# Optimization experiments

Hardware: AMD Instinct MI355X
Metric: run time of the kernel (lower is better)

Reference implementation:

```python
import jax, jax.numpy as jnp
import numpy as np

B = 1024          # batch
X = 32 * 32       # x_neuron_num
Y = 16384         # y_neuron_num (codebook size)
Z = 1000          # z_neuron_num (classes)
P_BU = 0.5        # y_bottom_up_percent


def _l2n(a, axis):
    # F.normalize: x / max(||x||, 1e-12)
    return a / jnp.maximum(jnp.linalg.norm(a, axis=axis, keepdims=True), 1e-12)


def setup_inputs() -> dict:
    key = jax.random.key(0)
    ks = jax.random.split(key, 8)
    return {
        "x": jax.random.normal(ks[0], (B, 32, 32), jnp.float32),
        "z": jax.random.randint(ks[1], (B,), 0, Z),
        "x2y_w": jax.random.uniform(ks[2], (Y, X), jnp.float32),
        "z2y_w": jax.random.uniform(ks[3], (Y, Z), jnp.float32),
        "y2z_w": jax.random.uniform(ks[4], (Z, Y), jnp.float32),
        "y_age": jax.random.randint(ks[5], (1, Y), 0, 5).astype(jnp.float32),
        "z_age": jax.random.randint(ks[6], (1, Z), 0, 5).astype(jnp.float32),
        "y_threshold": jax.random.uniform(ks[7], (1, Y), jnp.float32) * 0.5,
        "per_item": 1,
    }


def reference(x, z, x2y_w, z2y_w, y2z_w, y_age, z_age, y_threshold, per_item):
    # one 'train' step (torch forward returns inside the per_item loop)
    batch = x.shape[0]
    x = _l2n(x.reshape(batch, -1), 1)                 # [B, X]
    z_hot = jax.nn.one_hot(z, Z, dtype=x.dtype)       # normalized one-hot == one-hot
    Wx = _l2n(x2y_w, 1)                               # [Y, X]
    Wz = _l2n(z2y_w, 1)                               # [Y, Z]
    U = _l2n(y2z_w, 1)                                # [Z, Y]

    y_pre = P_BU * (x @ Wx.T) + (1.0 - P_BU) * (z_hot @ Wz.T)  # [B, Y]

    age = y_age[0]
    thr = y_threshold[0]
    max_resp = jnp.max(y_pre, axis=1)                 # [B]
    max_idx = jnp.argmax(y_pre, axis=1)               # [B]
    # age/threshold tie-break: losers re-argmax over unactivated neurons
    judge = (max_resp > thr[max_idx]) | (age[max_idx] < 1.0)
    unact = (age < 1.0).astype(y_pre.dtype)           # [Y]
    any_unact = jnp.sum(unact) > 0
    fallback = jnp.argmax(y_pre * unact[None, :], axis=1)
    max_idx = jnp.where(judge | ~any_unact, max_idx, fallback)

    # --- Hebbian update of x2y / z2y, expressed as segment reductions ---
    # torch dense form: sum_b y_lr[b,j]*(inp[b]-W[j]) / divisor_j
    ones_b = jnp.ones((batch,), x.dtype)
    cnt = jax.ops.segment_sum(ones_b, max_idx, num_segments=Y)       # [Y]
    div = jnp.where(cnt > 0, cnt, 1.0)
    lr = 1.0 / (age + 1.0)                                           # [Y]
    sumx = jax.ops.segment_sum(x, max_idx, num_segments=Y)           # [Y, X]
    Wx_new = Wx + (lr[:, None] * (sumx - cnt[:, None] * Wx)) / div[:, None]
    sumz = jax.ops.segment_sum(z_hot, max_idx, num_segments=Y)       # [Y, Z]
    Wz_new = Wz + (lr[:, None] * (sumz - cnt[:, None] * Wz)) / div[:, None]
    age_new = age + cnt

    # --- threshold update: per-winner min response (3 for non-winners) ---
    seg_min = jax.ops.segment_min(max_resp, max_idx, num_segments=Y)
    y_cur = jnp.minimum(seg_min, 3.0)
    y_cur = jnp.where(y_cur > 2.0, 0.0, y_cur)
    y_lr_eff = jnp.where(cnt > 0, lr, 0.0)   # sum_b y_lr[b,j]/divisor_j
    thr_new = y_lr_eff * y_cur + (1.0 - y_lr_eff) * thr

    # --- y2z update, segmented by label z ---
    zage = z_age[0]
    zlr = 1.0 / (zage + 1.0)                                          # [Z]
    y_resp = jax.nn.one_hot(max_idx, Y, dtype=x.dtype)                # [B, Y]
    cz = jax.ops.segment_sum(ones_b, z, num_segments=Z)               # [Z]
    dz = jnp.where(cz > 0, cz, 1.0)
    sumy = jax.ops.segment_sum(y_resp, z, num_segments=Z)             # [Z, Y]
    U_new = U + (zlr[:, None] * (sumy - cz[:, None] * U)) / dz[:, None]
    zage_new = zage + cz

    y_activated_num = jnp.sum((age_new >= 1.0).astype(jnp.int32))
    return (y_activated_num, max_resp, Wx_new, Wz_new, U_new,
            thr_new[None, :], age_new[None, :], zage_new[None, :])
```

## Files before the change

kernel.cpp:

```cpp
#include <hip/hip_runtime.h>

#define B_N 1024
#define X_N 1024
#define Y_N 16384
#define Z_N 1000
#define KD  1024
#define MARGIN 0.004f

#define OFF_ACT      0
#define OFF_MAXRESP  1
#define OFF_WX       1025
#define OFF_WZ       16778241
#define OFF_U        33162241
#define OFF_THR      49546241
#define OFF_AGE      49562625
#define OFF_ZAGE     49579009

#define SCR_B_BYTES    4112ull
#define SCR_S_BYTES    67112976ull
#define SCR_A_BYTES    132648976ull
#define SCR_CAND_BYTES 134746128ull
#define SCR_WZT_BYTES  136843280ull

#define WS_INV_X    0
#define WS_INV_WX   1024
#define WS_INV_WZ   17408
#define WS_FIDX     38912
#define WS_CNT      39936
#define WS_ZCNT     56320
#define WS_SEGMIN   57344
#define WS_CTR      73728
#define WS_MBITS    73736
#define WS_CCNT     74248

typedef unsigned short ushort_t;
typedef _Float16 f16x8 __attribute__((ext_vector_type(8)));
typedef float f32x4 __attribute__((ext_vector_type(4)));

__device__ __forceinline__ unsigned enc_f(float f) {
    unsigned u = __float_as_uint(f);
    return (u & 0x80000000u) ? ~u : (u | 0x80000000u);
}
__device__ __forceinline__ float dec_f(unsigned e) {
    unsigned u = (e & 0x80000000u) ? (e ^ 0x80000000u) : ~e;
    return __uint_as_float(u);
}
__device__ __forceinline__ unsigned long long pack_vi(float v, int y) {
    return ((unsigned long long)enc_f(v) << 32) |
           (unsigned long long)(0xFFFFFFFFu - (unsigned)y);
}
__device__ __forceinline__ ushort_t f2h(float f) {
    _Float16 h = (_Float16)f;
    ushort_t u; __builtin_memcpy(&u, &h, 2); return u;
}
__device__ __forceinline__ float h2f(unsigned lo16) {
    ushort_t u = (ushort_t)lo16; _Float16 h;
    __builtin_memcpy(&h, &u, 2); return (float)h;
}

#define GLOAD16(gp, lp) __builtin_amdgcn_global_load_lds( \
    (const __attribute__((address_space(1))) void*)(gp),  \
    (__attribute__((address_space(3))) void*)(lp), 16, 0, 0)

__global__ void init_kernel(int* cnt, unsigned* segmin, int* zcnt, int* ctr) {
    int i = blockIdx.x * 256 + threadIdx.x;
    if (i < Y_N) { cnt[i] = 0; segmin[i] = 0xFFFFFFFFu; }
    if (i < 1024) zcnt[i] = 0;
    if (i < 8) ctr[i] = (i == 2) ? 0x7FFFFFFF : 0;
}

__global__ void unact_kernel(const float* __restrict__ y_age, int* ctr,
                             unsigned long long* __restrict__ mbits) {
    int i = blockIdx.x * 256 + threadIdx.x;
    int a = (y_age[i] < 1.0f) ? 1 : 0;
    unsigned long long m = __ballot(a);
    int mi = a ? 0x7FFFFFFF : i;
    #pragma unroll
    for (int s = 32; s > 0; s >>= 1) mi = min(mi, __shfl_xor(mi, s, 64));
    if ((threadIdx.x & 63) == 0) {
        atomicAdd(ctr, (int)__popcll(m));
        mbits[i >> 6] = m;
        if (mi != 0x7FFFFFFF) atomicMin(&ctr[2], mi);
    }
}

__global__ __launch_bounds__(256) void pack_x_kernel(
    const float* __restrict__ x, ushort_t* __restrict__ A, float* __restrict__ inv_x) {
    const int b = blockIdx.x, t = threadIdx.x;
    const int lane = t & 63, wid = t >> 6;
    float4 v = reinterpret_cast<const float4*>(x + (size_t)b * X_N)[t];
    float ss = v.x*v.x + v.y*v.y + v.z*v.z + v.w*v.w;
    #pragma unroll
    for (int s = 32; s > 0; s >>= 1) ss += __shfl_xor(ss, s, 64);
    __shared__ float red[4];
    if (lane == 0) red[wid] = ss;
    __syncthreads();
    float inv = 1.0f / fmaxf(sqrtf(red[0] + red[1] + red[2] + red[3]), 1e-12f);
    if (t == 0) inv_x[b] = inv;
    ushort_t o1[4] = { f2h(v.x*inv), f2h(v.y*inv), f2h(v.z*inv), f2h(v.w*inv) };
    *reinterpret_cast<uint2*>(A + (size_t)b * KD + t * 4) = *reinterpret_cast<uint2*>(o1);
}

__global__ __launch_bounds__(256) void pack_w_kernel(
    const float* __restrict__ wxw, const float* __restrict__ wzw,
    ushort_t* __restrict__ Bm, float* __restrict__ inv_wx, float* __restrict__ inv_wz) {
    const int y = blockIdx.x, t = threadIdx.x;
    const int lane = t & 63, wid = t >> 6;
    float4 a = reinterpret_cast<const float4*>(wxw + (size_t)y * X_N)[t];
    float4 zv = make_float4(0.f, 0.f, 0.f, 0.f);
    if (t < 250) zv = reinterpret_cast<const float4*>(wzw + (size_t)y * Z_N)[t];
    float s1 = a.x*a.x + a.y*a.y + a.z*a.z + a.w*a.w;
    float s2 = zv.x*zv.x + zv.y*zv.y + zv.z*zv.z + zv.w*zv.w;
    #pragma unroll
    for (int s = 32; s > 0; s >>= 1) {
        s1 += __shfl_xor(s1, s, 64);
        s2 += __shfl_xor(s2, s, 64);
    }
    __shared__ float r1[4], r2[4];
    if (lane == 0) { r1[wid] = s1; r2[wid] = s2; }
    __syncthreads();
    float inv1 = 1.0f / fmaxf(sqrtf(r1[0] + r1[1] + r1[2] + r1[3]), 1e-12f);
    float inv2 = 1.0f / fmaxf(sqrtf(r2[0] + r2[1] + r2[2] + r2[3]), 1e-12f);
    ushort_t o1[4] = { f2h(a.x*inv1), f2h(a.y*inv1), f2h(a.z*inv1), f2h(a.w*inv1) };
    *reinterpret_cast<uint2*>(Bm + (size_t)y * KD + t * 4) = *reinterpret_cast<uint2*>(o1);
    if (t == 0) { inv_wx[y] = inv1; inv_wz[y] = inv2; }
}

__global__ __launch_bounds__(256) void wzt_kernel(
    const float* __restrict__ wzw, const float* __restrict__ inv_wz,
    ushort_t* __restrict__ wzt) {
    const int bid = blockIdx.x;
    const int z0 = (bid & 15) * 64, y0 = (bid >> 4) * 64;
    const int t = threadIdx.x;
    __shared__ float tile[64][65];
    #pragma unroll
    for (int p = 0; p < 4; ++p) {
        int yr = p * 16 + (t >> 4);
        int z = z0 + (t & 15) * 4;
        float4 v = make_float4(0.f, 0.f, 0.f, 0.f);
        if (z + 3 < Z_N)
            v = *reinterpret_cast<const float4*>(wzw + (size_t)(y0 + yr) * Z_N + z);
        float s = 0.5f * inv_wz[y0 + yr];
        tile[(t & 15) * 4 + 0][yr] = v.x * s;
        tile[(t & 15) * 4 + 1][yr] = v.y * s;
        tile[(t & 15) * 4 + 2][yr] = v.z * s;
        tile[(t & 15) * 4 + 3][yr] = v.w * s;
    }
    __syncthreads();
    #pragma unroll
    for (int p = 0; p < 4; ++p) {
        int zr = p * 16 + (t >> 4);
        int yc = (t & 15) * 4;
        if (z0 + zr < 1024) {
            ushort_t o[4] = { f2h(tile[zr][yc]), f2h(tile[zr][yc + 1]),
                              f2h(tile[zr][yc + 2]), f2h(tile[zr][yc + 3]) };
            *reinterpret_cast<uint2*>(wzt + (size_t)(z0 + zr) * Y_N + y0 + yc) =
                *reinterpret_cast<uint2*>(o);
        }
    }
}

__global__ __launch_bounds__(512, 1) void mm256_kernel(const ushort_t* __restrict__ A,
                                                       const ushort_t* __restrict__ Bm,
                                                       ushort_t* __restrict__ S) {
    __shared__ __align__(16) _Float16 lds[4][2][1024][8];
    const int t = threadIdx.x;
    const int wid = t >> 6, lane = t & 63;
    const int bid = blockIdx.x;
    const int lb = (bid & 7) * 32 + (bid >> 3);
    const int mt = lb & 3, nt = lb >> 2;
    const int b0 = mt * 256, y0 = nt * 256;
    const int wr = wid >> 2, wc = wid & 3;
    const int r = lane & 15, gq = lane >> 4;
    const int NK = KD / 32;

    f32x4 acc[8][4];
    #pragma unroll
    for (int i = 0; i < 8; ++i)
        #pragma unroll
        for (int j = 0; j < 4; ++j) acc[i][j] = (f32x4){0.f, 0.f, 0.f, 0.f};

    auto stage = [&](int buf, int k0) {
        #pragma unroll
        for (int rr = 0; rr < 2; ++rr) {
            int s = rr * 512 + t;
            int row = s & 255, g = s >> 8;
            GLOAD16(A  + (size_t)(b0 + row) * KD + k0 + g * 8, &lds[buf][0][s][0]);
            GLOAD16(Bm + (size_t)(y0 + row) * KD + k0 + g * 8, &lds[buf][1][s][0]);
        }
    };

    stage(0, 0);
    stage(1, 32);
    stage(2, 64);
    asm volatile("s_waitcnt vmcnt(8)" ::: "memory");
    __builtin_amdgcn_s_barrier();
    asm volatile("" ::: "memory");

    for (int ks = 0; ks < NK; ++ks) {
        const int cur = ks & 3;
        f16x8 bF[4];
        #pragma unroll
        for (int nf = 0; nf < 4; ++nf)
            bF[nf] = *reinterpret_cast<const f16x8*>(
                &lds[cur][1][gq * 256 + wc * 64 + nf * 16 + r][0]);
        __builtin_amdgcn_s_setprio(1);
        #pragma unroll
        for (int mf = 0; mf < 8; ++mf) {
            f16x8 aF = *reinterpret_cast<const f16x8*>(
                &lds[cur][0][gq * 256 + wr * 128 + mf * 16 + r][0]);
            #pragma unroll
            for (int nf = 0; nf < 4; ++nf)
                acc[mf][nf] = __builtin_amdgcn_mfma_f32_16x16x32_f16(
                    aF, bF[nf], acc[mf][nf], 0, 0, 0);
        }
        __builtin_amdgcn_s_setprio(0);
        if (ks == NK - 1) break;

        __builtin_amdgcn_s_barrier();
        asm volatile("" ::: "memory");
        if (ks + 3 < NK) {
            stage((ks + 3) & 3, (ks + 3) * 32);
            asm volatile("s_waitcnt vmcnt(8)" ::: "memory");
        } else if (ks + 3 == NK) {
            asm volatile("s_waitcnt vmcnt(4)" ::: "memory");
        } else {
            asm volatile("s_waitcnt vmcnt(0)" ::: "memory");
        }
        __builtin_amdgcn_s_barrier();
        asm volatile("" ::: "memory");
    }

    #pragma unroll
    for (int mf = 0; mf < 8; ++mf) {
        int bg = b0 + wr * 128 + mf * 16 + gq * 4;
        #pragma unroll
        for (int nf = 0; nf < 4; ++nf) {
            int yg = y0 + wc * 64 + nf * 16 + r;
            f32x4 c = acc[mf][nf];
            #pragma unroll
            for (int q = 0; q < 4; ++q)
                S[(size_t)(bg + q) * Y_N + yg] = f2h(0.5f * c[q]);
        }
    }
}

__global__ __launch_bounds__(256) void scan_kernel(
    const ushort_t* __restrict__ scores, const ushort_t* __restrict__ wzt,
    const int* __restrict__ zlab, const unsigned long long* __restrict__ mbits,
    const int* __restrict__ ctr, unsigned* __restrict__ gcand, int* __restrict__ ccnt) {
    const int b = blockIdx.x, t = threadIdx.x;
    const int lane = t & 63, wid = t >> 6;
    const uint4* srow = reinterpret_cast<const uint4*>(scores + (size_t)b * Y_N);
    const uint4* wrow = reinterpret_cast<const uint4*>(wzt + (size_t)zlab[b] * Y_N);

    float vmax = -1e30f, mmax = -1e30f;
    for (int c = t; c < Y_N / 8; c += 256) {
        uint4 pk = srow[c];
        uint4 wz = wrow[c];
        int yb = c * 8;
        unsigned m8 = (unsigned)((mbits[yb >> 6] >> (yb & 63)) & 0xFFull);
        unsigned w[4] = {pk.x, pk.y, pk.z, pk.w};
        unsigned q[4] = {wz.x, wz.y, wz.z, wz.w};
        #pragma unroll
        for (int j = 0; j < 4; ++j) {
            float v0 = h2f(w[j] & 0xFFFFu) + h2f(q[j] & 0xFFFFu);
            float v1 = h2f(w[j] >> 16) + h2f(q[j] >> 16);
            vmax = fmaxf(vmax, fmaxf(v0, v1));
            mmax = fmaxf(mmax, v0 * (float)((m8 >> (2 * j)) & 1u));
            mmax = fmaxf(mmax, v1 * (float)((m8 >> (2 * j + 1)) & 1u));
        }
    }
    #pragma unroll
    for (int s = 32; s > 0; s >>= 1) {
        vmax = fmaxf(vmax, __shfl_xor(vmax, s, 64));
        mmax = fmaxf(mmax, __shfl_xor(mmax, s, 64));
    }
    __shared__ float rv[4], rm[4];
    __shared__ int nA_s, nB_s;
    __shared__ int cA[256], cB[256];
    if (lane == 0) { rv[wid] = vmax; rm[wid] = mmax; }
    if (t == 0) { nA_s = 0; nB_s = 0; }
    __syncthreads();
    float tA = fmaxf(fmaxf(rv[0], rv[1]), fmaxf(rv[2], rv[3])) - MARGIN;
    float tB = fmaxf(fmaxf(rm[0], rm[1]), fmaxf(rm[2], rm[3])) - MARGIN;
    bool anyu = ctr[0] > 0;

    for (int c = t; c < Y_N / 8; c += 256) {
        uint4 pk = srow[c];
        uint4 wz = wrow[c];
        int yb = c * 8;
        unsigned m8 = (unsigned)((mbits[yb >> 6] >> (yb & 63)) & 0xFFull);
        unsigned w[4] = {pk.x, pk.y, pk.z, pk.w};
        unsigned q[4] = {wz.x, wz.y, wz.z, wz.w};
        #pragma unroll
        for (int j = 0; j < 8; ++j) {
            unsigned sw = (j & 1) ? (w[j >> 1] >> 16) : (w[j >> 1] & 0xFFFFu);
            unsigned qw = (j & 1) ? (q[j >> 1] >> 16) : (q[j >> 1] & 0xFFFFu);
            float v = h2f(sw) + h2f(qw);
            if (v >= tA) { int p = atomicAdd(&nA_s, 1); if (p < 256) cA[p] = yb + j; }
            if (anyu && ((m8 >> j) & 1u) && v >= tB) {
                int p = atomicAdd(&nB_s, 1); if (p < 256) cB[p] = yb + j;
            }
        }
    }
    __syncthreads();
    int nA = min(nA_s, 256), nB = min(nB_s, 256);
    unsigned* slab = gcand + (size_t)b * 512;
    for (int i = t; i < nA; i += 256) slab[i] = (unsigned)cA[i];
    for (int i = t; i < nB; i += 256) slab[256 + i] = (unsigned)cB[i];
    if (t == 0) ccnt[b] = nA | (nB << 16);
}

__global__ __launch_bounds__(256) void rescore_kernel(
    const unsigned* __restrict__ gcand, const int* __restrict__ ccnt,
    const float* __restrict__ x, const float* __restrict__ inv_x,
    const float* __restrict__ wxw, const float* __restrict__ inv_wx,
    const float* __restrict__ wzw, const float* __restrict__ inv_wz,
    const int* __restrict__ zlab, const float* __restrict__ y_thr,
    const float* __restrict__ y_age, const int* __restrict__ ctr,
    int* final_idx, int* cnt, unsigned* segmin, int* zcnt,
    float* __restrict__ out_maxresp) {
    const int b = blockIdx.x, t = threadIdx.x;
    const int lane = t & 63, wid = t >> 6;
    int pc = ccnt[b];
    int nA = pc & 0xFFFF, nB = pc >> 16;
    int zb = zlab[b];
    float invx = inv_x[b];
    const unsigned* slab = gcand + (size_t)b * 512;

    const float4* xr = reinterpret_cast<const float4*>(x + (size_t)b * X_N);
    float4 xv[4];
    #pragma unroll
    for (int j = 0; j < 4; ++j) xv[j] = xr[j * 64 + lane];

    __shared__ unsigned long long red[4];
    __shared__ unsigned long long sPM;
    __shared__ int sTakeA;

    unsigned long long bA = 0ull;
    for (int c = wid; c < nA; c += 8) {
        int y1 = (int)slab[c];
        int c2 = c + 4;
        bool h2 = c2 < nA;
        int y2 = (int)slab[h2 ? c2 : c];
        const float4* w1 = reinterpret_cast<const float4*>(wxw + (size_t)y1 * X_N);
        const float4* w2 = reinterpret_cast<const float4*>(wxw + (size_t)y2 * X_N);
        float d1 = 0.f, d2 = 0.f;
        #pragma unroll
        for (int j = 0; j < 4; ++j) {
            float4 a1 = w1[j * 64 + lane];
            float4 a2 = w2[j * 64 + lane];
            d1 += xv[j].x*a1.x + xv[j].y*a1.y + xv[j].z*a1.z + xv[j].w*a1.w;
            d2 += xv[j].x*a2.x + xv[j].y*a2.y + xv[j].z*a2.z + xv[j].w*a2.w;
        }
        #pragma unroll
        for (int s = 32; s > 0; s >>= 1) {
            d1 += __shfl_xor(d1, s, 64);
            d2 += __shfl_xor(d2, s, 64);
        }
        float v1 = 0.5f*invx*inv_wx[y1]*d1 + 0.5f*inv_wz[y1]*wzw[(size_t)y1*Z_N + zb];
        unsigned long long p1 = pack_vi(v1, y1);
        bA = (p1 > bA) ? p1 : bA;
        if (h2) {
            float v2 = 0.5f*invx*inv_wx[y2]*d2 + 0.5f*inv_wz[y2]*wzw[(size_t)y2*Z_N + zb];
            unsigned long long p2 = pack_vi(v2, y2);
            bA = (p2 > bA) ? p2 : bA;
        }
    }
    if (lane == 0) red[wid] = bA;
    __syncthreads();
    if (t == 0) {
        unsigned long long pm = red[0];
        #pragma unroll
        for (int j = 1; j < 4; ++j) pm = (red[j] > pm) ? red[j] : pm;
        sPM = pm;
        unsigned enc = (unsigned)(pm >> 32);
        int idx = (int)(0xFFFFFFFFu - (unsigned)(pm & 0xFFFFFFFFull));
        float mresp = dec_f(enc);
        out_maxresp[b] = mresp;
        bool judge = (mresp > y_thr[idx]) || (y_age[idx] < 1.0f);
        bool anyu = ctr[0] > 0;
        sTakeA = (judge || !anyu) ? 1 : 0;
    }
    __syncthreads();

    if (!sTakeA) {
        unsigned long long bB = 0ull;
        for (int c = wid; c < nB; c += 8) {
            int y1 = (int)slab[256 + c];
            int c2 = c + 4;
            bool h2 = c2 < nB;
            int y2 = (int)slab[256 + (h2 ? c2 : c)];
            const float4* w1 = reinterpret_cast<const float4*>(wxw + (size_t)y1 * X_N);
            const float4* w2 = reinterpret_cast<const float4*>(wxw + (size_t)y2 * X_N);
            float d1 = 0.f, d2 = 0.f;
            #pragma unroll
            for (int j = 0; j < 4; ++j) {
                float4 a1 = w1[j * 64 + lane];
                float4 a2 = w2[j * 64 + lane];
                d1 += xv[j].x*a1.x + xv[j].y*a1.y + xv[j].z*a1.z + xv[j].w*a1.w;
                d2 += xv[j].x*a2.x + xv[j].y*a2.y + xv[j].z*a2.z + xv[j].w*a2.w;
            }
            #pragma unroll
            for (int s = 32; s > 0; s >>= 1) {
                d1 += __shfl_xor(d1, s, 64);
                d2 += __shfl_xor(d2, s, 64);
            }
            float v1 = 0.5f*invx*inv_wx[y1]*d1 + 0.5f*inv_wz[y1]*wzw[(size_t)y1*Z_N + zb];
            unsigned long long p1 = pack_vi(v1, y1);
            bB = (p1 > bB) ? p1 : bB;
            if (h2) {
                float v2 = 0.5f*invx*inv_wx[y2]*d2 + 0.5f*inv_wz[y2]*wzw[(size_t)y2*Z_N + zb];
                unsigned long long p2 = pack_vi(v2, y2);
                bB = (p2 > bB) ? p2 : bB;
            }
        }
        if (lane == 0) red[wid] = bB;
    }
    __syncthreads();
    if (t == 0) {
        unsigned long long pm = sPM;
        unsigned enc = (unsigned)(pm >> 32);
        int idx = (int)(0xFFFFFFFFu - (unsigned)(pm & 0xFFFFFFFFull));
        int fin;
        if (sTakeA) {
            fin = idx;
        } else if (nB > 0) {
            unsigned long long pf = red[0];
            #pragma unroll
            for (int j = 1; j < 4; ++j) pf = (red[j] > pf) ? red[j] : pf;
            fin = (int)(0xFFFFFFFFu - (unsigned)(pf & 0xFFFFFFFFull));
        } else {
            fin = ctr[2];
        }
        final_idx[b] = fin;
        atomicAdd(&cnt[fin], 1);
        atomicMin(&segmin[fin], enc);
        atomicAdd(&zcnt[zb], 1);
    }
}

__global__ __launch_bounds__(256) void wx_out_kernel(
    const float* __restrict__ wxw, const float* __restrict__ inv_wx,
    const float* __restrict__ x, const float* __restrict__ inv_x,
    const int* __restrict__ final_idx, const int* __restrict__ cnt,
    const float* __restrict__ y_age, float* __restrict__ outw) {
    int j = blockIdx.x;
    int t = threadIdx.x;
    __shared__ int s_b[1024];
    __shared__ int s_n;
    if (t == 0) s_n = 0;
    __syncthreads();
    int c = cnt[j];
    if (c > 0) {
        for (int b = t; b < B_N; b += 256)
            if (final_idx[b] == j) { int p = atomicAdd(&s_n, 1); s_b[p] = b; }
    }
    __syncthreads();
    float inv = inv_wx[j];
    float lr = 1.0f / (y_age[j] + 1.0f);
    float fc = (float)c;
    float dv = (c > 0) ? fc : 1.0f;
    int n = s_n;
    float4 w = *reinterpret_cast<const float4*>(wxw + (size_t)j * X_N + t * 4);
    float4 wn = make_float4(w.x*inv, w.y*inv, w.z*inv, w.w*inv);
    if (c > 0) {
        float4 s = make_float4(0.f, 0.f, 0.f, 0.f);
        for (int m = 0; m < n; ++m) {
            int b = s_b[m];
            float ix = inv_x[b];
            float4 xv = *reinterpret_cast<const float4*>(x + (size_t)b * X_N + t * 4);
            s.x += xv.x * ix; s.y += xv.y * ix; s.z += xv.z * ix; s.w += xv.w * ix;
        }
        float f = lr / dv;
        wn.x += f * (s.x - fc * wn.x);
        wn.y += f * (s.y - fc * wn.y);
        wn.z += f * (s.z - fc * wn.z);
        wn.w += f * (s.w - fc * wn.w);
    }
    *reinterpret_cast<float4*>(outw + (size_t)j * X_N + t * 4) = wn;
}

__global__ __launch_bounds__(256) void wz_out_kernel(
    const float* __restrict__ wzw, const float* __restrict__ inv_wz,
    const int* __restrict__ zlab, const int* __restrict__ final_idx,
    const int* __restrict__ cnt, const float* __restrict__ y_age,
    float* __restrict__ outw) {
    int j = blockIdx.x;
    int t = threadIdx.x;
    __shared__ int s_c[1024];
    __shared__ int s_n;
    if (t == 0) s_n = 0;
    __syncthreads();
    int c = cnt[j];
    if (c > 0) {
        for (int b = t; b < B_N; b += 256)
            if (final_idx[b] == j) { int p = atomicAdd(&s_n, 1); s_c[p] = zlab[b]; }
    }
    __syncthreads();
    if (t >= 250) return;
    float inv = inv_wz[j];
    float lr = 1.0f / (y_age[j] + 1.0f);
    float fc = (float)c;
    float dv = (c > 0) ? fc : 1.0f;
    int n = s_n;
    float4 w = *reinterpret_cast<const float4*>(wzw + (size_t)j * Z_N + t * 4);
    float4 wn = make_float4(w.x*inv, w.y*inv, w.z*inv, w.w*inv);
    if (c > 0) {
        float4 s = make_float4(0.f, 0.f, 0.f, 0.f);
        for (int m = 0; m < n; ++m) {
            int d = s_c[m] - t * 4;
            if (d == 0) s.x += 1.f;
            else if (d == 1) s.y += 1.f;
            else if (d == 2) s.z += 1.f;
            else if (d == 3) s.w += 1.f;
        }
        float f = lr / dv;
        wn.x += f * (s.x - fc * wn.x);
        wn.y += f * (s.y - fc * wn.y);
        wn.z += f * (s.z - fc * wn.z);
        wn.w += f * (s.w - fc * wn.w);
    }
    *reinterpret_cast<float4*>(outw + (size_t)j * Z_N + t * 4) = wn;
}

__global__ __launch_bounds__(256) void u_out_kernel(
    const float* __restrict__ uw, const int* __restrict__ zlab,
    const int* __restrict__ final_idx, const int* __restrict__ zcnt,
    const float* __restrict__ z_age, float* __restrict__ outw) {
    int cz = blockIdx.x;
    int t = threadIdx.x;
    const int lane = t & 63, wid = t >> 6;
    __shared__ int s_w[1024];
    __shared__ int s_n;
    __shared__ float rss[4];
    if (t == 0) s_n = 0;

    const float4* rowp4 = reinterpret_cast<const float4*>(uw + (size_t)cz * Y_N);
    float4 u[16];
    float ss = 0.f;
    #pragma unroll
    for (int p = 0; p < 16; ++p) {
        u[p] = rowp4[p * 256 + t];
        ss += u[p].x*u[p].x + u[p].y*u[p].y + u[p].z*u[p].z + u[p].w*u[p].w;
    }
    #pragma unroll
    for (int s = 32; s > 0; s >>= 1) ss += __shfl_xor(ss, s, 64);
    if (lane == 0) rss[wid] = ss;
    __syncthreads();
    float inv = 1.0f / fmaxf(sqrtf(rss[0] + rss[1] + rss[2] + rss[3]), 1e-12f);

    int c = zcnt[cz];
    if (c > 0) {
        for (int b = t; b < B_N; b += 256)
            if (zlab[b] == cz) { int p = atomicAdd(&s_n, 1); s_w[p] = final_idx[b]; }
    }
    __syncthreads();
    float zlr = 1.0f / (z_age[cz] + 1.0f);
    float fc = (float)c;
    float dv = (c > 0) ? fc : 1.0f;
    float f = zlr / dv;
    int n = s_n;
    float* outp = outw + (size_t)cz * Y_N;
    #pragma unroll
    for (int p = 0; p < 16; ++p) {
        int e4 = p * 256 + t;
        float4 un = make_float4(u[p].x*inv, u[p].y*inv, u[p].z*inv, u[p].w*inv);
        if (c > 0) {
            float4 s = make_float4(0.f, 0.f, 0.f, 0.f);
            for (int m = 0; m < n; ++m) {
                int d = s_w[m] - e4 * 4;
                if (d == 0) s.x += 1.f;
                else if (d == 1) s.y += 1.f;
                else if (d == 2) s.z += 1.f;
                else if (d == 3) s.w += 1.f;
            }
            un.x += f * (s.x - fc * un.x);
            un.y += f * (s.y - fc * un.y);
            un.z += f * (s.z - fc * un.z);
            un.w += f * (s.w - fc * un.w);
        }
        *reinterpret_cast<float4*>(outp + e4 * 4) = un;
    }
}

__global__ void thr_age_kernel(const int* __restrict__ cnt, const unsigned* __restrict__ segmin,
                               const float* __restrict__ y_age, const float* __restrict__ y_thr,
                               float* __restrict__ out_thr, float* __restrict__ out_age,
                               int* ctr) {
    int j = blockIdx.x * 256 + threadIdx.x;
    int c = cnt[j];
    float age = y_age[j];
    float thr = y_thr[j];
    float tn = thr;
    if (c > 0) {
        float lr = 1.0f / (age + 1.0f);
        float smin = dec_f(segmin[j]);
        float ycur = fminf(smin, 3.0f);
        if (ycur > 2.0f) ycur = 0.0f;
        tn = lr * ycur + (1.0f - lr) * thr;
    }
    out_thr[j] = tn;
    float an = age + (float)c;
    out_age[j] = an;
    unsigned long long m = __ballot(an >= 1.0f ? 1 : 0);
    if ((threadIdx.x & 63) == 0) atomicAdd(ctr + 1, (int)__popcll(m));
}

__global__ void zage_act_kernel(const int* __restrict__ zcnt, const float* __restrict__ z_age,
                                const int* __restrict__ ctr, float* __restrict__ out_zage,
                                float* __restrict__ out_act) {
    int i = blockIdx.x * 256 + threadIdx.x;
    if (i < Z_N) out_zage[i] = z_age[i] + (float)zcnt[i];
    if (i == 0) out_act[0] = (float)ctr[1];
}

extern "C" void kernel_launch(void* const* d_in, const int* in_sizes, int n_in,
                              void* d_out, int out_size, void* d_ws, size_t ws_size,
                              hipStream_t stream) {
    const float* x     = (const float*)d_in[0];
    const int*   z     = (const int*)d_in[1];
    const float* wxw   = (const float*)d_in[2];
    const float* wzw   = (const float*)d_in[3];
    const float* uw    = (const float*)d_in[4];
    const float* y_age = (const float*)d_in[5];
    const float* z_age = (const float*)d_in[6];
    const float* y_thr = (const float*)d_in[7];
    float* out = (float*)d_out;
    float* ws  = (float*)d_ws;
    char*  ob  = (char*)d_out;

    float* inv_x  = ws + WS_INV_X;
    float* inv_wx = ws + WS_INV_WX;
    float* inv_wz = ws + WS_INV_WZ;
    int* fidx = (int*)(ws + WS_FIDX);
    int* cnt  = (int*)(ws + WS_CNT);
    int* zcnt = (int*)(ws + WS_ZCNT);
    unsigned* segmin = (unsigned*)(ws + WS_SEGMIN);
    int* ctr = (int*)(ws + WS_CTR);
    unsigned long long* mbits = (unsigned long long*)(ws + WS_MBITS);
    int* ccnt = (int*)(ws + WS_CCNT);

    ushort_t* Bb  = (ushort_t*)(ob + SCR_B_BYTES);
    ushort_t* Sc  = (ushort_t*)(ob + SCR_S_BYTES);
    ushort_t* Ab  = (ushort_t*)(ob + SCR_A_BYTES);
    unsigned* gcand = (unsigned*)(ob + SCR_CAND_BYTES);
    ushort_t* wzt = (ushort_t*)(ob + SCR_WZT_BYTES);

    init_kernel<<<64, 256, 0, stream>>>(cnt, segmin, zcnt, ctr);
    unact_kernel<<<Y_N / 256, 256, 0, stream>>>(y_age, ctr, mbits);
    pack_x_kernel<<<B_N, 256, 0, stream>>>(x, Ab, inv_x);
    pack_w_kernel<<<Y_N, 256, 0, stream>>>(wxw, wzw, Bb, inv_wx, inv_wz);
    wzt_kernel<<<16 * 256, 256, 0, stream>>>(wzw, inv_wz, wzt);
    mm256_kernel<<<(B_N / 256) * (Y_N / 256), 512, 0, stream>>>(Ab, Bb, Sc);
    scan_kernel<<<B_N, 256, 0, stream>>>(Sc, wzt, z, mbits, ctr, gcand, ccnt);
    rescore_kernel<<<B_N, 256, 0, stream>>>(gcand, ccnt, x, inv_x, wxw, inv_wx, wzw, inv_wz,
                                            z, y_thr, y_age, ctr, fidx, cnt, segmin, zcnt,
                                            out + OFF_MAXRESP);
    wx_out_kernel<<<Y_N, 256, 0, stream>>>(wxw, inv_wx, x, inv_x, fidx, cnt, y_age, out + OFF_WX);
    wz_out_kernel<<<Y_N, 256, 0, stream>>>(wzw, inv_wz, z, fidx, cnt, y_age, out + OFF_WZ);
    u_out_kernel<<<Z_N, 256, 0, stream>>>(uw, z, fidx, zcnt, z_age, out + OFF_U);
    thr_age_kernel<<<Y_N / 256, 256, 0, stream>>>(cnt, segmin, y_age, y_thr,
                                                  out + OFF_THR, out + OFF_AGE, ctr);
    zage_act_kernel<<<4, 256, 0, stream>>>(zcnt, z_age, ctr, out + OFF_ZAGE, out + OFF_ACT);
}
```

Before: 259.0 us.

## Fuse prep, scan/rescore and output kernels to cut launches and scratch traffic

Three groups of kernels are merged into block-indexed fused kernels. The unact, pack_x and pack_w work becomes one prep kernel. The scan and rescore kernels become one kernel that keeps candidate lists in shared memory instead of a global slab. The wx/wz/u output updates and the thr/age/zage work become one out kernel, and the activated-count write moves to a tiny final kernel. The aim is to remove per-launch gaps and tail serialization, and to skip the global candidate write and read. The trade-off is larger kernels with more shared memory and registers, which could lower occupancy, and heterogeneous block types whose run times differ.

```diff
diff --git a/kernel.cpp b/kernel.cpp
--- a/kernel.cpp
+++ b/kernel.cpp
@@ -19,7 +19,6 @@
 #define SCR_B_BYTES    4112ull
 #define SCR_S_BYTES    67112976ull
 #define SCR_A_BYTES    132648976ull
-#define SCR_CAND_BYTES 134746128ull
 #define SCR_WZT_BYTES  136843280ull
 
 #define WS_INV_X    0
@@ -31,7 +30,6 @@
 #define WS_SEGMIN   57344
 #define WS_CTR      73728
 #define WS_MBITS    73736
-#define WS_CCNT     74248
 
 typedef unsigned short ushort_t;
 typedef _Float16 f16x8 __attribute__((ext_vector_type(8)));
@@ -69,61 +67,59 @@
     if (i < 8) ctr[i] = (i == 2) ? 0x7FFFFFFF : 0;
 }
 
-__global__ void unact_kernel(const float* __restrict__ y_age, int* ctr,
-                             unsigned long long* __restrict__ mbits) {
-    int i = blockIdx.x * 256 + threadIdx.x;
-    int a = (y_age[i] < 1.0f) ? 1 : 0;
-    unsigned long long m = __ballot(a);
-    int mi = a ? 0x7FFFFFFF : i;
-    #pragma unroll
-    for (int s = 32; s > 0; s >>= 1) mi = min(mi, __shfl_xor(mi, s, 64));
-    if ((threadIdx.x & 63) == 0) {
-        atomicAdd(ctr, (int)__popcll(m));
-        mbits[i >> 6] = m;
-        if (mi != 0x7FFFFFFF) atomicMin(&ctr[2], mi);
-    }
-}
-
-__global__ __launch_bounds__(256) void pack_x_kernel(
-    const float* __restrict__ x, ushort_t* __restrict__ A, float* __restrict__ inv_x) {
-    const int b = blockIdx.x, t = threadIdx.x;
-    const int lane = t & 63, wid = t >> 6;
-    float4 v = reinterpret_cast<const float4*>(x + (size_t)b * X_N)[t];
-    float ss = v.x*v.x + v.y*v.y + v.z*v.z + v.w*v.w;
-    #pragma unroll
-    for (int s = 32; s > 0; s >>= 1) ss += __shfl_xor(ss, s, 64);
-    __shared__ float red[4];
-    if (lane == 0) red[wid] = ss;
-    __syncthreads();
-    float inv = 1.0f / fmaxf(sqrtf(red[0] + red[1] + red[2] + red[3]), 1e-12f);
-    if (t == 0) inv_x[b] = inv;
-    ushort_t o1[4] = { f2h(v.x*inv), f2h(v.y*inv), f2h(v.z*inv), f2h(v.w*inv) };
-    *reinterpret_cast<uint2*>(A + (size_t)b * KD + t * 4) = *reinterpret_cast<uint2*>(o1);
-}
-
-__global__ __launch_bounds__(256) void pack_w_kernel(
+__global__ __launch_bounds__(256) void prep_kernel(
+    const float* __restrict__ y_age, int* ctr, unsigned long long* __restrict__ mbits,
+    const float* __restrict__ x, ushort_t* __restrict__ A, float* __restrict__ inv_x,
     const float* __restrict__ wxw, const float* __restrict__ wzw,
     ushort_t* __restrict__ Bm, float* __restrict__ inv_wx, float* __restrict__ inv_wz) {
-    const int y = blockIdx.x, t = threadIdx.x;
+    const int bid = blockIdx.x, t = threadIdx.x;
     const int lane = t & 63, wid = t >> 6;
-    float4 a = reinterpret_cast<const float4*>(wxw + (size_t)y * X_N)[t];
-    float4 zv = make_float4(0.f, 0.f, 0.f, 0.f);
-    if (t < 250) zv = reinterpret_cast<const float4*>(wzw + (size_t)y * Z_N)[t];
-    float s1 = a.x*a.x + a.y*a.y + a.z*a.z + a.w*a.w;
-    float s2 = zv.x*zv.x + zv.y*zv.y + zv.z*zv.z + zv.w*zv.w;
-    #pragma unroll
-    for (int s = 32; s > 0; s >>= 1) {
-        s1 += __shfl_xor(s1, s, 64);
-        s2 += __shfl_xor(s2, s, 64);
-    }
-    __shared__ float r1[4], r2[4];
-    if (lane == 0) { r1[wid] = s1; r2[wid] = s2; }
-    __syncthreads();
-    float inv1 = 1.0f / fmaxf(sqrtf(r1[0] + r1[1] + r1[2] + r1[3]), 1e-12f);
-    float inv2 = 1.0f / fmaxf(sqrtf(r2[0] + r2[1] + r2[2] + r2[3]), 1e-12f);
-    ushort_t o1[4] = { f2h(a.x*inv1), f2h(a.y*inv1), f2h(a.z*inv1), f2h(a.w*inv1) };
-    *reinterpret_cast<uint2*>(Bm + (size_t)y * KD + t * 4) = *reinterpret_cast<uint2*>(o1);
-    if (t == 0) { inv_wx[y] = inv1; inv_wz[y] = inv2; }
+    __shared__ float red1[4], red2[4];
+
+    if (bid < 64) {
+        int i = bid * 256 + t;
+        int a = (y_age[i] < 1.0f) ? 1 : 0;
+        unsigned long long m = __ballot(a);
+        int mi = a ? 0x7FFFFFFF : i;
+        #pragma unroll
+        for (int s = 32; s > 0; s >>= 1) mi = min(mi, __shfl_xor(mi, s, 64));
+        if (lane == 0) {
+            atomicAdd(ctr, (int)__popcll(m));
+            mbits[i >> 6] = m;
+            if (mi != 0x7FFFFFFF) atomicMin(&ctr[2], mi);
+        }
+    } else if (bid < 64 + B_N) {
+        int b = bid - 64;
+        float4 v = reinterpret_cast<const float4*>(x + (size_t)b * X_N)[t];
+        float ss = v.x*v.x + v.y*v.y + v.z*v.z + v.w*v.w;
+        #pragma unroll
+        for (int s = 32; s > 0; s >>= 1) ss += __shfl_xor(ss, s, 64);
+        if (lane == 0) red1[wid] = ss;
+        __syncthreads();
+        float inv = 1.0f / fmaxf(sqrtf(red1[0] + red1[1] + red1[2] + red1[3]), 1e-12f);
+        if (t == 0) inv_x[b] = inv;
+        ushort_t o1[4] = { f2h(v.x*inv), f2h(v.y*inv), f2h(v.z*inv), f2h(v.w*inv) };
+        *reinterpret_cast<uint2*>(A + (size_t)b * KD + t * 4) = *reinterpret_cast<uint2*>(o1);
+    } else {
+        int y = bid - 64 - B_N;
+        float4 a = reinterpret_cast<const float4*>(wxw + (size_t)y * X_N)[t];
+        float4 zv = make_float4(0.f, 0.f, 0.f, 0.f);
+        if (t < 250) zv = reinterpret_cast<const float4*>(wzw + (size_t)y * Z_N)[t];
+        float s1 = a.x*a.x + a.y*a.y + a.z*a.z + a.w*a.w;
+        float s2 = zv.x*zv.x + zv.y*zv.y + zv.z*zv.z + zv.w*zv.w;
+        #pragma unroll
+        for (int s = 32; s > 0; s >>= 1) {
+            s1 += __shfl_xor(s1, s, 64);
+            s2 += __shfl_xor(s2, s, 64);
+        }
+        if (lane == 0) { red1[wid] = s1; red2[wid] = s2; }
+        __syncthreads();
+        float inv1 = 1.0f / fmaxf(sqrtf(red1[0] + red1[1] + red1[2] + red1[3]), 1e-12f);
+        float inv2 = 1.0f / fmaxf(sqrtf(red2[0] + red2[1] + red2[2] + red2[3]), 1e-12f);
+        ushort_t o1[4] = { f2h(a.x*inv1), f2h(a.y*inv1), f2h(a.z*inv1), f2h(a.w*inv1) };
+        *reinterpret_cast<uint2*>(Bm + (size_t)y * KD + t * 4) = *reinterpret_cast<uint2*>(o1);
+        if (t == 0) { inv_wx[y] = inv1; inv_wz[y] = inv2; }
+    }
 }
 
 __global__ __launch_bounds__(256) void wzt_kernel(
@@ -245,14 +241,28 @@
     }
 }
 
-__global__ __launch_bounds__(256) void scan_kernel(
+__global__ __launch_bounds__(256) void scanres_kernel(
     const ushort_t* __restrict__ scores, const ushort_t* __restrict__ wzt,
     const int* __restrict__ zlab, const unsigned long long* __restrict__ mbits,
-    const int* __restrict__ ctr, unsigned* __restrict__ gcand, int* __restrict__ ccnt) {
+    const int* __restrict__ ctr,
+    const float* __restrict__ x, const float* __restrict__ inv_x,
+    const float* __restrict__ wxw, const float* __restrict__ inv_wx,
+    const float* __restrict__ wzw, const float* __restrict__ inv_wz,
+    const float* __restrict__ y_thr, const float* __restrict__ y_age,
+    int* final_idx, int* cnt, unsigned* segmin, int* zcnt,
+    float* __restrict__ out_maxresp) {
     const int b = blockIdx.x, t = threadIdx.x;
     const int lane = t & 63, wid = t >> 6;
+    const int zb = zlab[b];
     const uint4* srow = reinterpret_cast<const uint4*>(scores + (size_t)b * Y_N);
-    const uint4* wrow = reinterpret_cast<const uint4*>(wzt + (size_t)zlab[b] * Y_N);
+    const uint4* wrow = reinterpret_cast<const uint4*>(wzt + (size_t)zb * Y_N);
+
+    __shared__ float rv[4], rm[4];
+    __shared__ int nA_s, nB_s;
+    __shared__ int cA[256], cB[256];
+    __shared__ unsigned long long red[4];
+    __shared__ unsigned long long sPM;
+    __shared__ int sTakeA;
 
     float vmax = -1e30f, mmax = -1e30f;
     for (int c = t; c < Y_N / 8; c += 256) {
@@ -276,9 +286,6 @@
         vmax = fmaxf(vmax, __shfl_xor(vmax, s, 64));
         mmax = fmaxf(mmax, __shfl_xor(mmax, s, 64));
     }
-    __shared__ float rv[4], rm[4];
-    __shared__ int nA_s, nB_s;
-    __shared__ int cA[256], cB[256];
     if (lane == 0) { rv[wid] = vmax; rm[wid] = mmax; }
     if (t == 0) { nA_s = 0; nB_s = 0; }
     __syncthreads();
@@ -306,44 +313,19 @@
     }
     __syncthreads();
     int nA = min(nA_s, 256), nB = min(nB_s, 256);
-    unsigned* slab = gcand + (size_t)b * 512;
-    for (int i = t; i < nA; i += 256) slab[i] = (unsigned)cA[i];
-    for (int i = t; i < nB; i += 256) slab[256 + i] = (unsigned)cB[i];
-    if (t == 0) ccnt[b] = nA | (nB << 16);
-}
-
-__global__ __launch_bounds__(256) void rescore_kernel(
-    const unsigned* __restrict__ gcand, const int* __restrict__ ccnt,
-    const float* __restrict__ x, const float* __restrict__ inv_x,
-    const float* __restrict__ wxw, const float* __restrict__ inv_wx,
-    const float* __restrict__ wzw, const float* __restrict__ inv_wz,
-    const int* __restrict__ zlab, const float* __restrict__ y_thr,
-    const float* __restrict__ y_age, const int* __restrict__ ctr,
-    int* final_idx, int* cnt, unsigned* segmin, int* zcnt,
-    float* __restrict__ out_maxresp) {
-    const int b = blockIdx.x, t = threadIdx.x;
-    const int lane = t & 63, wid = t >> 6;
-    int pc = ccnt[b];
-    int nA = pc & 0xFFFF, nB = pc >> 16;
-    int zb = zlab[b];
+
     float invx = inv_x[b];
-    const unsigned* slab = gcand + (size_t)b * 512;
-
     const float4* xr = reinterpret_cast<const float4*>(x + (size_t)b * X_N);
     float4 xv[4];
     #pragma unroll
     for (int j = 0; j < 4; ++j) xv[j] = xr[j * 64 + lane];
 
-    __shared__ unsigned long long red[4];
-    __shared__ unsigned long long sPM;
-    __shared__ int sTakeA;
-
     unsigned long long bA = 0ull;
     for (int c = wid; c < nA; c += 8) {
-        int y1 = (int)slab[c];
+        int y1 = cA[c];
         int c2 = c + 4;
         bool h2 = c2 < nA;
-        int y2 = (int)slab[h2 ? c2 : c];
+        int y2 = cA[h2 ? c2 : c];
         const float4* w1 = reinterpret_cast<const float4*>(wxw + (size_t)y1 * X_N);
         const float4* w2 = reinterpret_cast<const float4*>(wxw + (size_t)y2 * X_N);
         float d1 = 0.f, d2 = 0.f;
@@ -380,7 +362,6 @@
         float mresp = dec_f(enc);
         out_maxresp[b] = mresp;
         bool judge = (mresp > y_thr[idx]) || (y_age[idx] < 1.0f);
-        bool anyu = ctr[0] > 0;
         sTakeA = (judge || !anyu) ? 1 : 0;
     }
     __syncthreads();
@@ -388,10 +369,10 @@
     if (!sTakeA) {
         unsigned long long bB = 0ull;
         for (int c = wid; c < nB; c += 8) {
-            int y1 = (int)slab[256 + c];
+            int y1 = cB[c];
             int c2 = c + 4;
             bool h2 = c2 < nB;
-            int y2 = (int)slab[256 + (h2 ? c2 : c)];
+            int y2 = cB[h2 ? c2 : c];
             const float4* w1 = reinterpret_cast<const float4*>(wxw + (size_t)y1 * X_N);
             const float4* w2 = reinterpret_cast<const float4*>(wxw + (size_t)y2 * X_N);
             float d1 = 0.f, d2 = 0.f;
@@ -441,179 +422,161 @@
     }
 }
 
-__global__ __launch_bounds__(256) void wx_out_kernel(
+__global__ __launch_bounds__(256) void out_kernel(
     const float* __restrict__ wxw, const float* __restrict__ inv_wx,
     const float* __restrict__ x, const float* __restrict__ inv_x,
+    const float* __restrict__ wzw, const float* __restrict__ inv_wz,
+    const float* __restrict__ uw, const int* __restrict__ zlab,
     const int* __restrict__ final_idx, const int* __restrict__ cnt,
-    const float* __restrict__ y_age, float* __restrict__ outw) {
-    int j = blockIdx.x;
-    int t = threadIdx.x;
-    __shared__ int s_b[1024];
-    __shared__ int s_n;
-    if (t == 0) s_n = 0;
-    __syncthreads();
-    int c = cnt[j];
-    if (c > 0) {
-        for (int b = t; b < B_N; b += 256)
-            if (final_idx[b] == j) { int p = atomicAdd(&s_n, 1); s_b[p] = b; }
-    }
-    __syncthreads();
-    float inv = inv_wx[j];
-    float lr = 1.0f / (y_age[j] + 1.0f);
-    float fc = (float)c;
-    float dv = (c > 0) ? fc : 1.0f;
-    int n = s_n;
-    float4 w = *reinterpret_cast<const float4*>(wxw + (size_t)j * X_N + t * 4);
-    float4 wn = make_float4(w.x*inv, w.y*inv, w.z*inv, w.w*inv);
-    if (c > 0) {
-        float4 s = make_float4(0.f, 0.f, 0.f, 0.f);
-        for (int m = 0; m < n; ++m) {
-            int b = s_b[m];
-            float ix = inv_x[b];
-            float4 xv = *reinterpret_cast<const float4*>(x + (size_t)b * X_N + t * 4);
-            s.x += xv.x * ix; s.y += xv.y * ix; s.z += xv.z * ix; s.w += xv.w * ix;
-        }
-        float f = lr / dv;
-        wn.x += f * (s.x - fc * wn.x);
-        wn.y += f * (s.y - fc * wn.y);
-        wn.z += f * (s.z - fc * wn.z);
-        wn.w += f * (s.w - fc * wn.w);
-    }
-    *reinterpret_cast<float4*>(outw + (size_t)j * X_N + t * 4) = wn;
-}
-
-__global__ __launch_bounds__(256) void wz_out_kernel(
-    const float* __restrict__ wzw, const float* __restrict__ inv_wz,
-    const int* __restrict__ zlab, const int* __restrict__ final_idx,
-    const int* __restrict__ cnt, const float* __restrict__ y_age,
-    float* __restrict__ outw) {
-    int j = blockIdx.x;
-    int t = threadIdx.x;
-    __shared__ int s_c[1024];
-    __shared__ int s_n;
-    if (t == 0) s_n = 0;
-    __syncthreads();
-    int c = cnt[j];
-    if (c > 0) {
-        for (int b = t; b < B_N; b += 256)
-            if (final_idx[b] == j) { int p = atomicAdd(&s_n, 1); s_c[p] = zlab[b]; }
-    }
-    __syncthreads();
-    if (t >= 250) return;
-    float inv = inv_wz[j];
-    float lr = 1.0f / (y_age[j] + 1.0f);
-    float fc = (float)c;
-    float dv = (c > 0) ? fc : 1.0f;
-    int n = s_n;
-    float4 w = *reinterpret_cast<const float4*>(wzw + (size_t)j * Z_N + t * 4);
-    float4 wn = make_float4(w.x*inv, w.y*inv, w.z*inv, w.w*inv);
-    if (c > 0) {
-        float4 s = make_float4(0.f, 0.f, 0.f, 0.f);
-        for (int m = 0; m < n; ++m) {
-            int d = s_c[m] - t * 4;
-            if (d == 0) s.x += 1.f;
-            else if (d == 1) s.y += 1.f;
-            else if (d == 2) s.z += 1.f;
-            else if (d == 3) s.w += 1.f;
-        }
-        float f = lr / dv;
-        wn.x += f * (s.x - fc * wn.x);
-        wn.y += f * (s.y - fc * wn.y);
-        wn.z += f * (s.z - fc * wn.z);
-        wn.w += f * (s.w - fc * wn.w);
-    }
-    *reinterpret_cast<float4*>(outw + (size_t)j * Z_N + t * 4) = wn;
-}
-
-__global__ __launch_bounds__(256) void u_out_kernel(
-    const float* __restrict__ uw, const int* __restrict__ zlab,
-    const int* __restrict__ final_idx, const int* __restrict__ zcnt,
-    const float* __restrict__ z_age, float* __restrict__ outw) {
-    int cz = blockIdx.x;
-    int t = threadIdx.x;
+    const int* __restrict__ zcnt, const unsigned* __restrict__ segmin,
+    const float* __restrict__ y_age, const float* __restrict__ z_age,
+    const float* __restrict__ y_thr, float* __restrict__ out, int* ctr) {
+    const int bid = blockIdx.x, t = threadIdx.x;
     const int lane = t & 63, wid = t >> 6;
-    __shared__ int s_w[1024];
+    __shared__ int s_idx[1024];
     __shared__ int s_n;
     __shared__ float rss[4];
-    if (t == 0) s_n = 0;
-
-    const float4* rowp4 = reinterpret_cast<const float4*>(uw + (size_t)cz * Y_N);
-    float4 u[16];
-    float ss = 0.f;
-    #pragma unroll
-    for (int p = 0; p < 16; ++p) {
-        u[p] = rowp4[p * 256 + t];
-        ss += u[p].x*u[p].x + u[p].y*u[p].y + u[p].z*u[p].z + u[p].w*u[p].w;
-    }
-    #pragma unroll
-    for (int s = 32; s > 0; s >>= 1) ss += __shfl_xor(ss, s, 64);
-    if (lane == 0) rss[wid] = ss;
-    __syncthreads();
-    float inv = 1.0f / fmaxf(sqrtf(rss[0] + rss[1] + rss[2] + rss[3]), 1e-12f);
-
-    int c = zcnt[cz];
-    if (c > 0) {
-        for (int b = t; b < B_N; b += 256)
-            if (zlab[b] == cz) { int p = atomicAdd(&s_n, 1); s_w[p] = final_idx[b]; }
-    }
-    __syncthreads();
-    float zlr = 1.0f / (z_age[cz] + 1.0f);
-    float fc = (float)c;
-    float dv = (c > 0) ? fc : 1.0f;
-    float f = zlr / dv;
-    int n = s_n;
-    float* outp = outw + (size_t)cz * Y_N;
-    #pragma unroll
-    for (int p = 0; p < 16; ++p) {
-        int e4 = p * 256 + t;
-        float4 un = make_float4(u[p].x*inv, u[p].y*inv, u[p].z*inv, u[p].w*inv);
+
+    if (bid < Z_N) {
+        int cz = bid;
+        if (t == 0) s_n = 0;
+        const float4* rowp4 = reinterpret_cast<const float4*>(uw + (size_t)cz * Y_N);
+        float4 u[16];
+        float ss = 0.f;
+        #pragma unroll
+        for (int p = 0; p < 16; ++p) {
+            u[p] = rowp4[p * 256 + t];
+            ss += u[p].x*u[p].x + u[p].y*u[p].y + u[p].z*u[p].z + u[p].w*u[p].w;
+        }
+        #pragma unroll
+        for (int s = 32; s > 0; s >>= 1) ss += __shfl_xor(ss, s, 64);
+        if (lane == 0) rss[wid] = ss;
+        __syncthreads();
+        float inv = 1.0f / fmaxf(sqrtf(rss[0] + rss[1] + rss[2] + rss[3]), 1e-12f);
+        int c = zcnt[cz];
+        if (c > 0) {
+            for (int b = t; b < B_N; b += 256)
+                if (zlab[b] == cz) { int p = atomicAdd(&s_n, 1); s_idx[p] = final_idx[b]; }
+        }
+        __syncthreads();
+        float zlr = 1.0f / (z_age[cz] + 1.0f);
+        float fc = (float)c;
+        float dv = (c > 0) ? fc : 1.0f;
+        float f = zlr / dv;
+        int n = s_n;
+        float* outp = out + OFF_U + (size_t)cz * Y_N;
+        #pragma unroll
+        for (int p = 0; p < 16; ++p) {
+            int e4 = p * 256 + t;
+            float4 un = make_float4(u[p].x*inv, u[p].y*inv, u[p].z*inv, u[p].w*inv);
+            if (c > 0) {
+                float4 s = make_float4(0.f, 0.f, 0.f, 0.f);
+                for (int m = 0; m < n; ++m) {
+                    int d = s_idx[m] - e4 * 4;
+                    if (d == 0) s.x += 1.f;
+                    else if (d == 1) s.y += 1.f;
+                    else if (d == 2) s.z += 1.f;
+                    else if (d == 3) s.w += 1.f;
+                }
+                un.x += f * (s.x - fc * un.x);
+                un.y += f * (s.y - fc * un.y);
+                un.z += f * (s.z - fc * un.z);
+                un.w += f * (s.w - fc * un.w);
+            }
+            *reinterpret_cast<float4*>(outp + e4 * 4) = un;
+        }
+    } else if (bid < Z_N + Y_N) {
+        int j = bid - Z_N;
+        if (t == 0) s_n = 0;
+        __syncthreads();
+        int c = cnt[j];
+        if (c > 0) {
+            for (int b = t; b < B_N; b += 256)
+                if (final_idx[b] == j) { int p = atomicAdd(&s_n, 1); s_idx[p] = b; }
+        }
+        __syncthreads();
+        float inv = inv_wx[j];
+        float lr = 1.0f / (y_age[j] + 1.0f);
+        float fc = (float)c;
+        float dv = (c > 0) ? fc : 1.0f;
+        int n = s_n;
+        float4 w = *reinterpret_cast<const float4*>(wxw + (size_t)j * X_N + t * 4);
+        float4 wn = make_float4(w.x*inv, w.y*inv, w.z*inv, w.w*inv);
         if (c > 0) {
             float4 s = make_float4(0.f, 0.f, 0.f, 0.f);
             for (int m = 0; m < n; ++m) {
-                int d = s_w[m] - e4 * 4;
+                int b = s_idx[m];
+                float ix = inv_x[b];
+                float4 xv = *reinterpret_cast<const float4*>(x + (size_t)b * X_N + t * 4);
+                s.x += xv.x * ix; s.y += xv.y * ix; s.z += xv.z * ix; s.w += xv.w * ix;
+            }
+            float f = lr / dv;
+            wn.x += f * (s.x - fc * wn.x);
+            wn.y += f * (s.y - fc * wn.y);
+            wn.z += f * (s.z - fc * wn.z);
+            wn.w += f * (s.w - fc * wn.w);
+        }
+        *reinterpret_cast<float4*>(out + OFF_WX + (size_t)j * X_N + t * 4) = wn;
+    } else if (bid < Z_N + 2 * Y_N) {
+        int j = bid - Z_N - Y_N;
+        if (t == 0) s_n = 0;
+        __syncthreads();
+        int c = cnt[j];
+        if (c > 0) {
+            for (int b = t; b < B_N; b += 256)
+                if (final_idx[b] == j) { int p = atomicAdd(&s_n, 1); s_idx[p] = zlab[b]; }
+        }
+        __syncthreads();
+        if (t >= 250) return;
+        float inv = inv_wz[j];
+        float lr = 1.0f / (y_age[j] + 1.0f);
+        float fc = (float)c;
+        float dv = (c > 0) ? fc : 1.0f;
+        int n = s_n;
+        float4 w = *reinterpret_cast<const float4*>(wzw + (size_t)j * Z_N + t * 4);
+        float4 wn = make_float4(w.x*inv, w.y*inv, w.z*inv, w.w*inv);
+        if (c > 0) {
+            float4 s = make_float4(0.f, 0.f, 0.f, 0.f);
+            for (int m = 0; m < n; ++m) {
+                int d = s_idx[m] - t * 4;
                 if (d == 0) s.x += 1.f;
                 else if (d == 1) s.y += 1.f;
                 else if (d == 2) s.z += 1.f;
                 else if (d == 3) s.w += 1.f;
             }
-            un.x += f * (s.x - fc * un.x);
-            un.y += f * (s.y - fc * un.y);
-            un.z += f * (s.z - fc * un.z);
-            un.w += f * (s.w - fc * un.w);
-        }
-        *reinterpret_cast<float4*>(outp + e4 * 4) = un;
-    }
-}
-
-__global__ void thr_age_kernel(const int* __restrict__ cnt, const unsigned* __restrict__ segmin,
-                               const float* __restrict__ y_age, const float* __restrict__ y_thr,
-                               float* __restrict__ out_thr, float* __restrict__ out_age,
-                               int* ctr) {
-    int j = blockIdx.x * 256 + threadIdx.x;
-    int c = cnt[j];
-    float age = y_age[j];
-    float thr = y_thr[j];
-    float tn = thr;
-    if (c > 0) {
-        float lr = 1.0f / (age + 1.0f);
-        float smin = dec_f(segmin[j]);
-        float ycur = fminf(smin, 3.0f);
-        if (ycur > 2.0f) ycur = 0.0f;
-        tn = lr * ycur + (1.0f - lr) * thr;
-    }
-    out_thr[j] = tn;
-    float an = age + (float)c;
-    out_age[j] = an;
-    unsigned long long m = __ballot(an >= 1.0f ? 1 : 0);
-    if ((threadIdx.x & 63) == 0) atomicAdd(ctr + 1, (int)__popcll(m));
-}
-
-__global__ void zage_act_kernel(const int* __restrict__ zcnt, const float* __restrict__ z_age,
-                                const int* __restrict__ ctr, float* __restrict__ out_zage,
-                                float* __restrict__ out_act) {
-    int i = blockIdx.x * 256 + threadIdx.x;
-    if (i < Z_N) out_zage[i] = z_age[i] + (float)zcnt[i];
-    if (i == 0) out_act[0] = (float)ctr[1];
+            float f = lr / dv;
+            wn.x += f * (s.x - fc * wn.x);
+            wn.y += f * (s.y - fc * wn.y);
+            wn.z += f * (s.z - fc * wn.z);
+            wn.w += f * (s.w - fc * wn.w);
+        }
+        *reinterpret_cast<float4*>(out + OFF_WZ + (size_t)j * Z_N + t * 4) = wn;
+    } else if (bid < Z_N + 2 * Y_N + 64) {
+        int j = (bid - Z_N - 2 * Y_N) * 256 + t;
+        int c = cnt[j];
+        float age = y_age[j];
+        float thr = y_thr[j];
+        float tn = thr;
+        if (c > 0) {
+            float lr = 1.0f / (age + 1.0f);
+            float smin = dec_f(segmin[j]);
+            float ycur = fminf(smin, 3.0f);
+            if (ycur > 2.0f) ycur = 0.0f;
+            tn = lr * ycur + (1.0f - lr) * thr;
+        }
+        out[OFF_THR + j] = tn;
+        float an = age + (float)c;
+        out[OFF_AGE + j] = an;
+        unsigned long long m = __ballot(an >= 1.0f ? 1 : 0);
+        if (lane == 0) atomicAdd(ctr + 1, (int)__popcll(m));
+    } else {
+        int i = (bid - Z_N - 2 * Y_N - 64) * 256 + t;
+        if (i < Z_N) out[OFF_ZAGE + i] = z_age[i] + (float)zcnt[i];
+    }
+}
+
+__global__ void act_kernel(const int* __restrict__ ctr, float* __restrict__ out_act) {
+    if (threadIdx.x == 0) out_act[0] = (float)ctr[1];
 }
 
 extern "C" void kernel_launch(void* const* d_in, const int* in_sizes, int n_in,
@@ -640,28 +603,22 @@
     unsigned* segmin = (unsigned*)(ws + WS_SEGMIN);
     int* ctr = (int*)(ws + WS_CTR);
     unsigned long long* mbits = (unsigned long long*)(ws + WS_MBITS);
-    int* ccnt = (int*)(ws + WS_CCNT);
 
     ushort_t* Bb  = (ushort_t*)(ob + SCR_B_BYTES);
     ushort_t* Sc  = (ushort_t*)(ob + SCR_S_BYTES);
     ushort_t* Ab  = (ushort_t*)(ob + SCR_A_BYTES);
-    unsigned* gcand = (unsigned*)(ob + SCR_CAND_BYTES);
     ushort_t* wzt = (ushort_t*)(ob + SCR_WZT_BYTES);
 
     init_kernel<<<64, 256, 0, stream>>>(cnt, segmin, zcnt, ctr);
-    unact_kernel<<<Y_N / 256, 256, 0, stream>>>(y_age, ctr, mbits);
-    pack_x_kernel<<<B_N, 256, 0, stream>>>(x, Ab, inv_x);
-    pack_w_kernel<<<Y_N, 256, 0, stream>>>(wxw, wzw, Bb, inv_wx, inv_wz);
+    prep_kernel<<<64 + B_N + Y_N, 256, 0, stream>>>(y_age, ctr, mbits, x, Ab, inv_x,
+                                                    wxw, wzw, Bb, inv_wx, inv_wz);
     wzt_kernel<<<16 * 256, 256, 0, stream>>>(wzw, inv_wz, wzt);
     mm256_kernel<<<(B_N / 256) * (Y_N / 256), 512, 0, stream>>>(Ab, Bb, Sc);
-    scan_kernel<<<B_N, 256, 0, stream>>>(Sc, wzt, z, mbits, ctr, gcand, ccnt);
-    rescore_kernel<<<B_N, 256, 0, stream>>>(gcand, ccnt, x, inv_x, wxw, inv_wx, wzw, inv_wz,
-                                            z, y_thr, y_age, ctr, fidx, cnt, segmin, zcnt,
-                                            out + OFF_MAXRESP);
-    wx_out_kernel<<<Y_N, 256, 0, stream>>>(wxw, inv_wx, x, inv_x, fidx, cnt, y_age, out + OFF_WX);
-    wz_out_kernel<<<Y_N, 256, 0, stream>>>(wzw, inv_wz, z, fidx, cnt, y_age, out + OFF_WZ);
-    u_out_kernel<<<Z_N, 256, 0, stream>>>(uw, z, fidx, zcnt, z_age, out + OFF_U);
-    thr_age_kernel<<<Y_N / 256, 256, 0, stream>>>(cnt, segmin, y_age, y_thr,
-                                                  out + OFF_THR, out + OFF_AGE, ctr);
-    zage_act_kernel<<<4, 256, 0, stream>>>(zcnt, z_age, ctr, out + OFF_ZAGE, out + OFF_ACT);
-}
+    scanres_kernel<<<B_N, 256, 0, stream>>>(Sc, wzt, z, mbits, ctr, x, inv_x,
+                                            wxw, inv_wx, wzw, inv_wz, y_thr, y_age,
+                                            fidx, cnt, segmin, zcnt, out + OFF_MAXRESP);
+    out_kernel<<<Z_N + 2 * Y_N + 64 + 4, 256, 0, stream>>>(
+        wxw, inv_wx, x, inv_x, wzw, inv_wz, uw, z, fidx, cnt, zcnt, segmin,
+        y_age, z_age, y_thr, out, ctr);
+    act_kernel<<<1, 64, 0, stream>>>(ctr, out + OFF_ACT);
+}
```

Result: faster. 235.8 us, median of 2 (-9.0%).
